# Kernel optimization log

Hardware: AMD Instinct MI355X
Metric: run time of the kernel (lower is better)

Reference implementation:

```python
import jax, jax.numpy as jnp
import numpy as np

NUM_HEADS = 12

def setup_inputs() -> dict:
    key = jax.random.key(0)
    k1, k2, k3 = jax.random.split(key, 3)
    B, H, W, C = 8, 32, 32, 768
    x = jax.random.normal(k1, (B, H, W, C), dtype=jnp.float32)
    qkv_w = jax.random.normal(k2, (3 * C, C), dtype=jnp.float32) * (C ** -0.5)
    qkv_b = jnp.zeros((3 * C,), dtype=jnp.float32)
    proj_w = jax.random.normal(k3, (C, C), dtype=jnp.float32) * (C ** -0.5)
    proj_b = jnp.zeros((C,), dtype=jnp.float32)
    return {"x": x, "qkv_w": qkv_w, "qkv_b": qkv_b, "proj_w": proj_w, "proj_b": proj_b}

def reference(x, qkv_w, qkv_b, proj_w, proj_b):
    B, H, W, C = x.shape
    N = H * W
    h = NUM_HEADS
    d = C // h
    scale = d ** -0.5
    xf = x.reshape(B, N, C)
    # fused QKV projection: [B,N,3C] -> [3,B,h,N,d]
    qkv = (xf @ qkv_w.T + qkv_b).reshape(B, N, 3, h, d).transpose(2, 0, 3, 1, 4)
    q, k, v = qkv[0], qkv[1], qkv[2]  # rope = Identity
    # scaled dot-product attention
    scores = jnp.einsum('bhnd,bhmd->bhnm', q, k) * scale
    attn = jax.nn.softmax(scores, axis=-1)
    out = jnp.einsum('bhnm,bhmd->bhnd', attn, v)
    out = out.transpose(0, 2, 1, 3).reshape(B, N, C)
    out = out @ proj_w.T + proj_b
    return out.reshape(B, H, W, C)
```

## Files before the change

kernel.cpp:

```cpp
#include <hip/hip_runtime.h>
#include <math.h>

#define AS1 __attribute__((address_space(1)))
#define AS3 __attribute__((address_space(3)))

typedef __attribute__((ext_vector_type(8))) short bf16x8;
typedef __attribute__((ext_vector_type(4))) float f32x4;

__device__ __forceinline__ unsigned short f2bf(float f) {
    union { float f; unsigned int i; } v; v.f = f;
    unsigned int r = v.i + 0x7FFFu + ((v.i >> 16) & 1u);
    return (unsigned short)(r >> 16);
}

__device__ __forceinline__ unsigned int pack2bf(float lo, float hi) {
    union { float f; unsigned int i; } a, b; a.f = lo; b.f = hi;
    return __builtin_amdgcn_perm(b.i + 0x8000u, a.i + 0x8000u, 0x07060302u);
}

#define NTOK 1024
#define CCH  768
#define HD   64
#define QKS  1536

#define N1C (8192 * 768 / 4)
#define N2C (2304 * 768 / 4)
#define N3C (768 * 768 / 4)

__global__ void cvt_all(const float* __restrict__ x, const float* __restrict__ w1,
                        const float* __restrict__ w2,
                        unsigned short* __restrict__ xb, unsigned short* __restrict__ w1b,
                        unsigned short* __restrict__ w2b)
{
    int i = blockIdx.x * blockDim.x + threadIdx.x;
    const float4* s; ushort4* d; int k;
    if (i < N1C)            { s = (const float4*)x;  d = (ushort4*)xb;  k = i; }
    else if (i < N1C + N2C) { s = (const float4*)w1; d = (ushort4*)w1b; k = i - N1C; }
    else if (i < N1C + N2C + N3C) { s = (const float4*)w2; d = (ushort4*)w2b; k = i - N1C - N2C; }
    else return;
    const float4 v = s[k];
    ushort4 o;
    o.x = f2bf(v.x); o.y = f2bf(v.y); o.z = f2bf(v.z); o.w = f2bf(v.w);
    d[k] = o;
}

#define PROJ_STAGE(t, buf) do {                                                              \
    __builtin_amdgcn_global_load_lds((AS1 void*)(Ag  + (t) * 32), (AS3 void*)(Asx[buf] + dstA),  16, 0, 0); \
    __builtin_amdgcn_global_load_lds((AS1 void*)(Wg0 + (t) * 32), (AS3 void*)(Bsx[buf] + dstB0), 16, 0, 0); \
    __builtin_amdgcn_global_load_lds((AS1 void*)(Wg1 + (t) * 32), (AS3 void*)(Bsx[buf] + dstB1), 16, 0, 0); \
  } while (0)

#define PROJ_STEP(cur) do {                                                                  \
    bf16x8 af[2], bfv[4];                                                                    \
    _Pragma("unroll")                                                                        \
    for (int i = 0; i < 2; ++i)                                                              \
        af[i] = *(const bf16x8*)((const char*)&Asx[0][0] + (cur) * 4096 + dA + i * 1024);    \
    _Pragma("unroll")                                                                        \
    for (int j = 0; j < 4; ++j)                                                              \
        bfv[j] = *(const bf16x8*)((const char*)&Bsx[0][0] + (cur) * 8192 + dB + j * 1024);   \
    __builtin_amdgcn_s_setprio(1);                                                           \
    _Pragma("unroll")                                                                        \
    for (int i = 0; i < 2; ++i)                                                              \
      _Pragma("unroll")                                                                      \
      for (int j = 0; j < 4; ++j)                                                            \
        acc[i][j] = __builtin_amdgcn_mfma_f32_16x16x32_bf16(af[i], bfv[j], acc[i][j], 0, 0, 0); \
    __builtin_amdgcn_s_setprio(0);                                                           \
  } while (0)

__global__ __launch_bounds__(256, 4)
void gemm_proj(const unsigned short* __restrict__ A,
               const unsigned short* __restrict__ W,
               const float* __restrict__ bias,
               float* __restrict__ Cmat)
{
    const int N = 768, K = 768;
    __shared__ __align__(16) unsigned short Asx[4][64 * 32];
    __shared__ __align__(16) unsigned short Bsx[4][128 * 32];

    const int tid  = threadIdx.x;
    const int wave = tid >> 6;
    const int lane = tid & 63;
    const int quad = lane >> 4;
    const int l15  = lane & 15;
    const int wr   = wave >> 1;
    const int wc   = wave & 1;

    const int lin = blockIdx.x;
    const int idx = (lin & 7) * 96 + (lin >> 3);
    const int mt  = idx / 6;
    const int nt  = idx % 6;
    const int m0  = mt * 64;
    const int n0  = nt * 128;

    const int r  = tid >> 2;
    const int sp = tid & 3;
    const int sl = sp ^ ((r >> 1) & 3);
    const unsigned short* Ag  = A + (size_t)(m0 + r)      * K + sl * 8;
    const unsigned short* Wg0 = W + (size_t)(n0 + r)      * K + sl * 8;
    const unsigned short* Wg1 = W + (size_t)(n0 + 64 + r) * K + sl * 8;
    const int dstA  = tid * 8;
    const int dstB0 = tid * 8;
    const int dstB1 = tid * 8 + 2048;

    int dA = (wr * 32 + l15) * 64 + quad * 16;
    dA ^= ((dA >> 7) & 1) << 4;  dA ^= ((dA >> 8) & 1) << 5;
    int dB = (wc * 64 + l15) * 64 + quad * 16;
    dB ^= ((dB >> 7) & 1) << 4;  dB ^= ((dB >> 8) & 1) << 5;

    f32x4 acc[2][4];
#pragma unroll
    for (int i = 0; i < 2; ++i)
#pragma unroll
        for (int j = 0; j < 4; ++j) acc[i][j] = (f32x4){0.f, 0.f, 0.f, 0.f};

    PROJ_STAGE(0, 0);
    PROJ_STAGE(1, 1);
    PROJ_STAGE(2, 2);
    asm volatile("s_waitcnt vmcnt(6)" ::: "memory");
    __builtin_amdgcn_s_barrier();
    __builtin_amdgcn_sched_barrier(0);

#pragma unroll
    for (int t = 0; t < 21; ++t) {
        PROJ_STAGE(t + 3, (t + 3) & 3);
        __builtin_amdgcn_sched_barrier(0);
        PROJ_STEP(t & 3);
        asm volatile("s_waitcnt vmcnt(6)" ::: "memory");
        __builtin_amdgcn_s_barrier();
        __builtin_amdgcn_sched_barrier(0);
    }
    PROJ_STEP(1);
    asm volatile("s_waitcnt vmcnt(3)" ::: "memory");
    __builtin_amdgcn_s_barrier();
    __builtin_amdgcn_sched_barrier(0);
    PROJ_STEP(2);
    asm volatile("s_waitcnt vmcnt(0)" ::: "memory");
    __builtin_amdgcn_s_barrier();
    __builtin_amdgcn_sched_barrier(0);
    PROJ_STEP(3);

#pragma unroll
    for (int i = 0; i < 2; ++i) {
        const int row = m0 + wr * 32 + i * 16 + quad * 4;
#pragma unroll
        for (int j = 0; j < 4; ++j) {
            const int col = n0 + wc * 64 + j * 16 + l15;
            const float bv = bias[col];
#pragma unroll
            for (int r2 = 0; r2 < 4; ++r2)
                Cmat[(size_t)(row + r2) * N + col] = acc[i][j][r2] + bv;
        }
    }
}

#define QKV_STAGE(t, buf) do {                                                               \
    __builtin_amdgcn_global_load_lds((AS1 void*)(Ag0 + (t) * 32), (AS3 void*)(As[buf] + dst0), 16, 0, 0); \
    __builtin_amdgcn_global_load_lds((AS1 void*)(Ag1 + (t) * 32), (AS3 void*)(As[buf] + dst1), 16, 0, 0); \
    __builtin_amdgcn_global_load_lds((AS1 void*)(Wg0 + (t) * 32), (AS3 void*)(Bs[buf] + dst0), 16, 0, 0); \
    __builtin_amdgcn_global_load_lds((AS1 void*)(Wg1 + (t) * 32), (AS3 void*)(Bs[buf] + dst1), 16, 0, 0); \
  } while (0)

#define QKV_STEP(cur) do {                                                                   \
    bf16x8 af[4], bfv[4];                                                                    \
    _Pragma("unroll")                                                                        \
    for (int i = 0; i < 4; ++i)                                                              \
        af[i] = *(const bf16x8*)((const char*)&As[0][0] + (cur) * 8192 + dA + i * 1024);     \
    _Pragma("unroll")                                                                        \
    for (int j = 0; j < 4; ++j)                                                              \
        bfv[j] = *(const bf16x8*)((const char*)&Bs[0][0] + (cur) * 8192 + dB + j * 1024);    \
    __builtin_amdgcn_s_setprio(1);                                                           \
    _Pragma("unroll")                                                                        \
    for (int i = 0; i < 4; ++i)                                                              \
      _Pragma("unroll")                                                                      \
      for (int j = 0; j < 4; ++j)                                                            \
        acc[i][j] = __builtin_amdgcn_mfma_f32_16x16x32_bf16(af[i], bfv[j], acc[i][j], 0, 0, 0); \
    __builtin_amdgcn_s_setprio(0);                                                           \
  } while (0)

__global__ __launch_bounds__(256, 2)
void gemm_qkv(const unsigned short* __restrict__ A,
              const unsigned short* __restrict__ W,
              const float* __restrict__ bias,
              unsigned short* __restrict__ qk,
              unsigned short* __restrict__ vT)
{
    const int K = 768;
    __shared__ __align__(16) unsigned short As[4][128 * 32];
    __shared__ __align__(16) unsigned short Bs[4][128 * 32];

    const int tid  = threadIdx.x;
    const int wave = tid >> 6;
    const int lane = tid & 63;
    const int quad = lane >> 4;
    const int l15  = lane & 15;
    const int wr   = wave >> 1;
    const int wc   = wave & 1;

    const int lin = blockIdx.x;
    const int idx = (lin & 7) * 144 + (lin >> 3);
    const int mt  = idx / 18;
    const int nt  = idx % 18;
    const int m0  = mt * 128;
    const int n0  = nt * 128;

    const int srow  = tid >> 2;
    const int scolb = ((tid & 3) << 4)
                    ^ (((tid >> 3) & 1) << 4)
                    ^ (((tid >> 4) & 1) << 5);
    const unsigned short* Ag0 = A + (size_t)(m0 + srow)      * K + (scolb >> 1);
    const unsigned short* Ag1 = A + (size_t)(m0 + 64 + srow) * K + (scolb >> 1);
    const unsigned short* Wg0 = W + (size_t)(n0 + srow)      * K + (scolb >> 1);
    const unsigned short* Wg1 = W + (size_t)(n0 + 64 + srow) * K + (scolb >> 1);
    const int dst0 = tid * 8;
    const int dst1 = tid * 8 + 2048;

    int dA = (wr * 64 + l15) * 64 + quad * 16;
    dA ^= ((dA >> 7) & 1) << 4;  dA ^= ((dA >> 8) & 1) << 5;
    int dB = (wc * 64 + l15) * 64 + quad * 16;
    dB ^= ((dB >> 7) & 1) << 4;  dB ^= ((dB >> 8) & 1) << 5;

    f32x4 acc[4][4];
#pragma unroll
    for (int i = 0; i < 4; ++i)
#pragma unroll
        for (int j = 0; j < 4; ++j) acc[i][j] = (f32x4){0.f, 0.f, 0.f, 0.f};

    QKV_STAGE(0, 0);
    QKV_STAGE(1, 1);
    QKV_STAGE(2, 2);
    asm volatile("s_waitcnt vmcnt(8)" ::: "memory");
    __builtin_amdgcn_s_barrier();
    __builtin_amdgcn_sched_barrier(0);

#pragma unroll
    for (int t = 0; t < 21; ++t) {
        QKV_STAGE(t + 3, (t + 3) & 3);
        __builtin_amdgcn_sched_barrier(0);
        QKV_STEP(t & 3);
        asm volatile("s_waitcnt vmcnt(8)" ::: "memory");
        __builtin_amdgcn_s_barrier();
        __builtin_amdgcn_sched_barrier(0);
    }
    QKV_STEP(1);
    asm volatile("s_waitcnt vmcnt(4)" ::: "memory");
    __builtin_amdgcn_s_barrier();
    __builtin_amdgcn_sched_barrier(0);
    QKV_STEP(2);
    asm volatile("s_waitcnt vmcnt(0)" ::: "memory");
    __builtin_amdgcn_s_barrier();
    __builtin_amdgcn_sched_barrier(0);
    QKV_STEP(3);

    const int colbase = n0 + wc * 64;
    if (colbase < 1536) {
        const float s = (colbase < 768) ? 0.125f : 1.f;
#pragma unroll
        for (int i = 0; i < 4; ++i) {
            const int row = m0 + wr * 64 + i * 16 + quad * 4;
#pragma unroll
            for (int j = 0; j < 4; ++j) {
                const int col = colbase + j * 16 + l15;
                const float bv = bias[col];
#pragma unroll
                for (int r = 0; r < 4; ++r)
                    qk[(size_t)(row + r) * QKS + col] = f2bf((acc[i][j][r] + bv) * s);
            }
        }
    } else {
#pragma unroll
        for (int i = 0; i < 4; ++i) {
            const int m    = m0 + wr * 64 + i * 16 + quad * 4;
            const int b    = m >> 10;
            const int tok  = m & 1023;
            const int tile = tok >> 6;
            const int K0   = tok & 63;
#pragma unroll
            for (int j = 0; j < 4; ++j) {
                const int col = colbase + j * 16 + l15;
                const int c   = col - 1536;
                const int h   = c >> 6, d = c & 63;
                const float bv = bias[col];
                const int bh     = b * 12 + h;
                const int region = (d >> 4) * 2 + (K0 >> 5);
                const int L      = ((K0 >> 3) & 3) * 16 + (d & 15);
                uint2 o;
                o.x = pack2bf(acc[i][j][0] + bv, acc[i][j][1] + bv);
                o.y = pack2bf(acc[i][j][2] + bv, acc[i][j][3] + bv);
                *(uint2*)(vT + (((size_t)(bh * 16 + tile) * 8 + region) << 9) + L * 8 + (K0 & 7)) = o;
            }
        }
    }
}

__global__ __launch_bounds__(256, 4)
void attn_fused(const unsigned short* __restrict__ qk,
                const unsigned short* __restrict__ vT,
                unsigned short* __restrict__ aout)
{
    __shared__ __align__(16) unsigned short Kf[2][8 * 512];
    __shared__ __align__(16) unsigned short Vt[2][8 * 512];
    __shared__ __align__(16) unsigned short Ps[8 * 512];

    const int tid  = threadIdx.x;
    const int wave = tid >> 6;
    const int lane = tid & 63;
    const int quad = lane >> 4;
    const int l15  = lane & 15;

    const int lin = blockIdx.x;
    const int bh  = lin % 96;
    const int qt  = lin / 96;
    const int b   = bh / 12;
    const int h   = bh % 12;

    const unsigned short* Qg  = qk + (size_t)b * NTOK * QKS + (size_t)h * HD;
    const unsigned short* Kg  = Qg + CCH;
    const unsigned short* vTb = vT + (size_t)bh * 16 * 8 * 512;

    const int q0 = qt * 128;

    bf16x8 qf[2][2];
#pragma unroll
    for (int qb = 0; qb < 2; ++qb)
#pragma unroll
        for (int ks = 0; ks < 2; ++ks)
            qf[qb][ks] = *(const bf16x8*)(Qg + (size_t)(q0 + wave * 32 + qb * 16 + l15) * QKS
                                              + ks * 32 + quad * 8);

    f32x4 oacc[2][4];
#pragma unroll
    for (int qb = 0; qb < 2; ++qb)
#pragma unroll
        for (int nb = 0; nb < 4; ++nb) oacc[qb][nb] = (f32x4){0.f, 0.f, 0.f, 0.f};
    float lrow[2] = {0.f, 0.f};

    const unsigned short* kdma = Kg + (size_t)(wave * 16 + l15) * QKS + quad * 8;

#pragma unroll
    for (int ks = 0; ks < 2; ++ks)
        __builtin_amdgcn_global_load_lds((AS1 void*)(kdma + ks * 32),
            (AS3 void*)(Kf[0] + (wave * 2 + ks) * 512 + lane * 8), 16, 0, 0);
#pragma unroll
    for (int u = 0; u < 2; ++u)
        __builtin_amdgcn_global_load_lds((AS1 void*)(vTb + (size_t)(wave * 2 + u) * 512 + lane * 8),
            (AS3 void*)(Vt[0] + (wave * 2 + u) * 512 + lane * 8), 16, 0, 0);

    for (int t = 0; t < 16; ++t) {
        const int cur = t & 1;
        __syncthreads();

        if (t < 15) {
            const int nxt = cur ^ 1;
#pragma unroll
            for (int ks = 0; ks < 2; ++ks)
                __builtin_amdgcn_global_load_lds((AS1 void*)(kdma + (size_t)((t + 1) * 64) * QKS + ks * 32),
                    (AS3 void*)(Kf[nxt] + (wave * 2 + ks) * 512 + lane * 8), 16, 0, 0);
#pragma unroll
            for (int u = 0; u < 2; ++u)
                __builtin_amdgcn_global_load_lds((AS1 void*)(vTb + ((size_t)(t + 1) * 8 + wave * 2 + u) * 512 + lane * 8),
                    (AS3 void*)(Vt[nxt] + (wave * 2 + u) * 512 + lane * 8), 16, 0, 0);
        }

        f32x4 sacc[2][4];
#pragma unroll
        for (int qb = 0; qb < 2; ++qb)
#pragma unroll
            for (int jk = 0; jk < 4; ++jk) sacc[qb][jk] = (f32x4){0.f, 0.f, 0.f, 0.f};
#pragma unroll
        for (int ks = 0; ks < 2; ++ks) {
            bf16x8 kf[4];
#pragma unroll
            for (int jk = 0; jk < 4; ++jk)
                kf[jk] = *(const bf16x8*)(Kf[cur] + (jk * 2 + ks) * 512 + lane * 8);
#pragma unroll
            for (int qb = 0; qb < 2; ++qb)
#pragma unroll
                for (int jk = 0; jk < 4; ++jk)
                    sacc[qb][jk] = __builtin_amdgcn_mfma_f32_16x16x32_bf16(
                        kf[jk], qf[qb][ks], sacc[qb][jk], 0, 0, 0);
        }

#pragma unroll
        for (int qb = 0; qb < 2; ++qb) {
            float rsum = 0.f;
#pragma unroll
            for (int jk = 0; jk < 4; ++jk)
#pragma unroll
                for (int r = 0; r < 4; ++r) {
                    const float p = __expf(sacc[qb][jk][r]);
                    sacc[qb][jk][r] = p;
                    rsum += p;
                }
            rsum += __shfl_xor(rsum, 16);
            rsum += __shfl_xor(rsum, 32);
            lrow[qb] += rsum;
        }

#pragma unroll
        for (int p = 0; p < 2; ++p) {
#pragma unroll
            for (int qb = 0; qb < 2; ++qb)
#pragma unroll
                for (int jh = 0; jh < 2; ++jh) {
                    const int jk = 2 * p + jh;
                    uint2 o;
                    o.x = pack2bf(sacc[qb][jk][0], sacc[qb][jk][1]);
                    o.y = pack2bf(sacc[qb][jk][2], sacc[qb][jk][3]);
                    const int off = (wave * 2 + qb) * 512
                                  + ((jh * 2 + (quad >> 1)) * 16 + l15) * 8 + (quad & 1) * 4;
                    *(uint2*)&Ps[off] = o;
                }
            bf16x8 pf[2], vf[4];
#pragma unroll
            for (int qb = 0; qb < 2; ++qb)
                pf[qb] = *(const bf16x8*)(Ps + (wave * 2 + qb) * 512 + lane * 8);
#pragma unroll
            for (int nb = 0; nb < 4; ++nb)
                vf[nb] = *(const bf16x8*)(Vt[cur] + (nb * 2 + p) * 512 + lane * 8);
#pragma unroll
            for (int qb = 0; qb < 2; ++qb)
#pragma unroll
                for (int nb = 0; nb < 4; ++nb)
                    oacc[qb][nb] = __builtin_amdgcn_mfma_f32_16x16x32_bf16(
                        vf[nb], pf[qb], oacc[qb][nb], 0, 0, 0);
        }
    }

#pragma unroll
    for (int qb = 0; qb < 2; ++qb) {
        const float inv = 1.f / lrow[qb];
        const size_t tok = (size_t)(b * NTOK + q0 + wave * 32 + qb * 16 + l15);
#pragma unroll
        for (int nb = 0; nb < 4; ++nb) {
            uint2 o;
            o.x = pack2bf(oacc[qb][nb][0] * inv, oacc[qb][nb][1] * inv);
            o.y = pack2bf(oacc[qb][nb][2] * inv, oacc[qb][nb][3] * inv);
            *(uint2*)(aout + tok * CCH + h * HD + nb * 16 + quad * 4) = o;
        }
    }
}

extern "C" void kernel_launch(void* const* d_in, const int* in_sizes, int n_in,
                              void* d_out, int out_size, void* d_ws, size_t ws_size,
                              hipStream_t stream)
{
    const float* x      = (const float*)d_in[0];
    const float* qkv_w  = (const float*)d_in[1];
    const float* qkv_b  = (const float*)d_in[2];
    const float* proj_w = (const float*)d_in[3];
    const float* proj_b = (const float*)d_in[4];
    float* out = (float*)d_out;

    unsigned short* qk  = (unsigned short*)d_ws;
    unsigned short* att = qk  + (size_t)8192 * 1536;
    unsigned short* xb  = att + (size_t)8192 * 768;
    unsigned short* wqb = xb  + (size_t)8192 * 768;
    unsigned short* wpb = wqb + (size_t)2304 * 768;
    unsigned short* vT  = wpb + (size_t)768 * 768;

    cvt_all<<<dim3((N1C + N2C + N3C + 255) / 256), dim3(256), 0, stream>>>(x, qkv_w, proj_w, xb, wqb, wpb);
    gemm_qkv<<<dim3(1152), dim3(256), 0, stream>>>(xb, wqb, qkv_b, qk, vT);
    attn_fused<<<dim3(768), dim3(256), 0, stream>>>(qk, vT, att);
    gemm_proj<<<dim3(768), dim3(256), 0, stream>>>(att, wpb, proj_b, out);
}
```

Baseline: 190.5 us.

## Retile QKV GEMM to 128x256 blocks with 8 waves and BK=64 triple buffering

The QKV projection GEMM now uses 512-thread blocks covering a 128x256 output tile, with a K step of 64 split into two half-steps. Shared memory is triple-buffered, and global-to-LDS loads are interleaved between the half-steps. The block-to-XCD mapping is also reworked. The aim is to reuse each A tile across more output columns and halve the number of barrier/pipeline iterations. In exchange, occupancy drops to one large block per CU and the LDS footprint grows, which may reduce latency hiding.

```diff
diff --git a/kernel.cpp b/kernel.cpp
--- a/kernel.cpp
+++ b/kernel.cpp
@@ -153,31 +153,19 @@
     }
 }
 
-#define QKV_STAGE(t, buf) do {                                                               \
-    __builtin_amdgcn_global_load_lds((AS1 void*)(Ag0 + (t) * 32), (AS3 void*)(As[buf] + dst0), 16, 0, 0); \
-    __builtin_amdgcn_global_load_lds((AS1 void*)(Ag1 + (t) * 32), (AS3 void*)(As[buf] + dst1), 16, 0, 0); \
-    __builtin_amdgcn_global_load_lds((AS1 void*)(Wg0 + (t) * 32), (AS3 void*)(Bs[buf] + dst0), 16, 0, 0); \
-    __builtin_amdgcn_global_load_lds((AS1 void*)(Wg1 + (t) * 32), (AS3 void*)(Bs[buf] + dst1), 16, 0, 0); \
+#define QKV_ST3a(t, buf) do {                                                                \
+    __builtin_amdgcn_global_load_lds((AS1 void*)(Ag  + (t) * 64),      (AS3 void*)(AsE + (buf) * 8192  + tid * 8), 16, 0, 0); \
+    __builtin_amdgcn_global_load_lds((AS1 void*)(Ag  + (t) * 64 + 32), (AS3 void*)(AsE + (buf) * 8192  + 4096 + tid * 8), 16, 0, 0); \
+    __builtin_amdgcn_global_load_lds((AS1 void*)(Wg0 + (t) * 64),      (AS3 void*)(BsE + (buf) * 16384 + tid * 8), 16, 0, 0); \
   } while (0)
 
-#define QKV_STEP(cur) do {                                                                   \
-    bf16x8 af[4], bfv[4];                                                                    \
-    _Pragma("unroll")                                                                        \
-    for (int i = 0; i < 4; ++i)                                                              \
-        af[i] = *(const bf16x8*)((const char*)&As[0][0] + (cur) * 8192 + dA + i * 1024);     \
-    _Pragma("unroll")                                                                        \
-    for (int j = 0; j < 4; ++j)                                                              \
-        bfv[j] = *(const bf16x8*)((const char*)&Bs[0][0] + (cur) * 8192 + dB + j * 1024);    \
-    __builtin_amdgcn_s_setprio(1);                                                           \
-    _Pragma("unroll")                                                                        \
-    for (int i = 0; i < 4; ++i)                                                              \
-      _Pragma("unroll")                                                                      \
-      for (int j = 0; j < 4; ++j)                                                            \
-        acc[i][j] = __builtin_amdgcn_mfma_f32_16x16x32_bf16(af[i], bfv[j], acc[i][j], 0, 0, 0); \
-    __builtin_amdgcn_s_setprio(0);                                                           \
+#define QKV_ST3b(t, buf) do {                                                                \
+    __builtin_amdgcn_global_load_lds((AS1 void*)(Wg1 + (t) * 64),      (AS3 void*)(BsE + (buf) * 16384 + 4096  + tid * 8), 16, 0, 0); \
+    __builtin_amdgcn_global_load_lds((AS1 void*)(Wg0 + (t) * 64 + 32), (AS3 void*)(BsE + (buf) * 16384 + 8192  + tid * 8), 16, 0, 0); \
+    __builtin_amdgcn_global_load_lds((AS1 void*)(Wg1 + (t) * 64 + 32), (AS3 void*)(BsE + (buf) * 16384 + 12288 + tid * 8), 16, 0, 0); \
   } while (0)
 
-__global__ __launch_bounds__(256, 2)
+__global__ __launch_bounds__(512, 1)
 void gemm_qkv(const unsigned short* __restrict__ A,
               const unsigned short* __restrict__ W,
               const float* __restrict__ bias,
@@ -185,36 +173,36 @@
               unsigned short* __restrict__ vT)
 {
     const int K = 768;
-    __shared__ __align__(16) unsigned short As[4][128 * 32];
-    __shared__ __align__(16) unsigned short Bs[4][128 * 32];
+    __shared__ __align__(16) unsigned short As[3 * 8192];
+    __shared__ __align__(16) unsigned short Bs[3 * 16384];
+    unsigned short* AsE = &As[0];
+    unsigned short* BsE = &Bs[0];
 
     const int tid  = threadIdx.x;
     const int wave = tid >> 6;
     const int lane = tid & 63;
     const int quad = lane >> 4;
     const int l15  = lane & 15;
-    const int wr   = wave >> 1;
-    const int wc   = wave & 1;
+    const int wm   = wave >> 2;
+    const int wc   = wave & 3;
 
     const int lin = blockIdx.x;
-    const int idx = (lin & 7) * 144 + (lin >> 3);
-    const int mt  = idx / 18;
-    const int nt  = idx % 18;
-    const int m0  = mt * 128;
-    const int n0  = nt * 128;
+    const int xcd = lin & 7;
+    const int j9  = lin >> 3;
+    const int bx  = xcd * 8 + j9 / 9;
+    const int by  = j9 % 9;
+    const int m0  = bx * 128;
+    const int n0  = by * 256;
 
     const int srow  = tid >> 2;
     const int scolb = ((tid & 3) << 4)
                     ^ (((tid >> 3) & 1) << 4)
                     ^ (((tid >> 4) & 1) << 5);
-    const unsigned short* Ag0 = A + (size_t)(m0 + srow)      * K + (scolb >> 1);
-    const unsigned short* Ag1 = A + (size_t)(m0 + 64 + srow) * K + (scolb >> 1);
-    const unsigned short* Wg0 = W + (size_t)(n0 + srow)      * K + (scolb >> 1);
-    const unsigned short* Wg1 = W + (size_t)(n0 + 64 + srow) * K + (scolb >> 1);
-    const int dst0 = tid * 8;
-    const int dst1 = tid * 8 + 2048;
-
-    int dA = (wr * 64 + l15) * 64 + quad * 16;
+    const unsigned short* Ag  = A + (size_t)(m0 + srow)       * K + (scolb >> 1);
+    const unsigned short* Wg0 = W + (size_t)(n0 + srow)       * K + (scolb >> 1);
+    const unsigned short* Wg1 = W + (size_t)(n0 + 128 + srow) * K + (scolb >> 1);
+
+    int dA = (wm * 64 + l15) * 64 + quad * 16;
     dA ^= ((dA >> 7) & 1) << 4;  dA ^= ((dA >> 8) & 1) << 5;
     int dB = (wc * 64 + l15) * 64 + quad * 16;
     dB ^= ((dB >> 7) & 1) << 4;  dB ^= ((dB >> 8) & 1) << 5;
@@ -225,38 +213,53 @@
 #pragma unroll
         for (int j = 0; j < 4; ++j) acc[i][j] = (f32x4){0.f, 0.f, 0.f, 0.f};
 
-    QKV_STAGE(0, 0);
-    QKV_STAGE(1, 1);
-    QKV_STAGE(2, 2);
-    asm volatile("s_waitcnt vmcnt(8)" ::: "memory");
+    QKV_ST3a(0, 0); QKV_ST3b(0, 0);
+    QKV_ST3a(1, 1); QKV_ST3b(1, 1);
+    asm volatile("s_waitcnt vmcnt(6)" ::: "memory");
     __builtin_amdgcn_s_barrier();
     __builtin_amdgcn_sched_barrier(0);
 
 #pragma unroll
-    for (int t = 0; t < 21; ++t) {
-        QKV_STAGE(t + 3, (t + 3) & 3);
-        __builtin_amdgcn_sched_barrier(0);
-        QKV_STEP(t & 3);
-        asm volatile("s_waitcnt vmcnt(8)" ::: "memory");
-        __builtin_amdgcn_s_barrier();
-        __builtin_amdgcn_sched_barrier(0);
-    }
-    QKV_STEP(1);
-    asm volatile("s_waitcnt vmcnt(4)" ::: "memory");
-    __builtin_amdgcn_s_barrier();
-    __builtin_amdgcn_sched_barrier(0);
-    QKV_STEP(2);
-    asm volatile("s_waitcnt vmcnt(0)" ::: "memory");
-    __builtin_amdgcn_s_barrier();
-    __builtin_amdgcn_sched_barrier(0);
-    QKV_STEP(3);
+    for (int t = 0; t < 12; ++t) {
+        const int buf = t % 3;
+#pragma unroll
+        for (int kh = 0; kh < 2; ++kh) {
+            bf16x8 af[4], bfv[4];
+#pragma unroll
+            for (int i = 0; i < 4; ++i)
+                af[i] = *(const bf16x8*)((const char*)AsE + buf * 16384 + kh * 8192 + dA + i * 1024);
+#pragma unroll
+            for (int j = 0; j < 4; ++j)
+                bfv[j] = *(const bf16x8*)((const char*)BsE + buf * 32768 + kh * 16384 + dB + j * 1024);
+            if (t < 10) {
+                if (kh == 0) QKV_ST3a(t + 2, (t + 2) % 3);
+                else         QKV_ST3b(t + 2, (t + 2) % 3);
+            }
+            __builtin_amdgcn_s_barrier();
+            asm volatile("s_waitcnt lgkmcnt(0)" ::: "memory");
+            __builtin_amdgcn_sched_barrier(0);
+            __builtin_amdgcn_s_setprio(1);
+#pragma unroll
+            for (int i = 0; i < 4; ++i)
+#pragma unroll
+                for (int j = 0; j < 4; ++j)
+                    acc[i][j] = __builtin_amdgcn_mfma_f32_16x16x32_bf16(af[i], bfv[j], acc[i][j], 0, 0, 0);
+            __builtin_amdgcn_s_setprio(0);
+            if (kh == 1) {
+                if (t < 10)       asm volatile("s_waitcnt vmcnt(6)" ::: "memory");
+                else if (t == 10) asm volatile("s_waitcnt vmcnt(0)" ::: "memory");
+            }
+            __builtin_amdgcn_s_barrier();
+            __builtin_amdgcn_sched_barrier(0);
+        }
+    }
 
     const int colbase = n0 + wc * 64;
     if (colbase < 1536) {
         const float s = (colbase < 768) ? 0.125f : 1.f;
 #pragma unroll
         for (int i = 0; i < 4; ++i) {
-            const int row = m0 + wr * 64 + i * 16 + quad * 4;
+            const int row = m0 + wm * 64 + i * 16 + quad * 4;
 #pragma unroll
             for (int j = 0; j < 4; ++j) {
                 const int col = colbase + j * 16 + l15;
@@ -269,7 +272,7 @@
     } else {
 #pragma unroll
         for (int i = 0; i < 4; ++i) {
-            const int m    = m0 + wr * 64 + i * 16 + quad * 4;
+            const int m    = m0 + wm * 64 + i * 16 + quad * 4;
             const int b    = m >> 10;
             const int tok  = m & 1023;
             const int tile = tok >> 6;
@@ -459,7 +462,7 @@
     unsigned short* vT  = wpb + (size_t)768 * 768;
 
     cvt_all<<<dim3((N1C + N2C + N3C + 255) / 256), dim3(256), 0, stream>>>(x, qkv_w, proj_w, xb, wqb, wpb);
-    gemm_qkv<<<dim3(1152), dim3(256), 0, stream>>>(xb, wqb, qkv_b, qk, vT);
+    gemm_qkv<<<dim3(576), dim3(512), 0, stream>>>(xb, wqb, qkv_b, qk, vT);
     attn_fused<<<dim3(768), dim3(256), 0, stream>>>(qk, vT, att);
     gemm_proj<<<dim3(768), dim3(256), 0, stream>>>(att, wpb, proj_b, out);
 }
```

New measurement: 196.9 us. 3.3% more time.
